# Kernel optimization log

Measured on AMD Instinct MI355X. Metric: run time of the kernel, lower is better.

## Reference

```python
import jax, jax.numpy as jnp
import numpy as np

B, T, D, E, K = 4, 2048, 1024, 8, 2

def setup_inputs() -> dict:
    key = jax.random.key(0)
    ks = jax.random.split(key, 4)
    scale = 1.0 / np.sqrt(D)
    return {
        "input_feat": jax.random.normal(ks[0], (B, T, D), dtype=jnp.float32),
        "delta": jax.random.normal(ks[1], (B, T, D), dtype=jnp.float32),
        "gate_W": jax.random.normal(ks[2], (E, D), dtype=jnp.float32) * scale,
        "gate_b": jnp.zeros((E,), dtype=jnp.float32),
        "expert_W": jax.random.normal(ks[3], (E, D, D), dtype=jnp.float32) * scale,
        "expert_b": jnp.zeros((E, D), dtype=jnp.float32),
    }

def reference(input_feat, delta, gate_W, gate_b, expert_W, expert_b):
    # Gating: logits [B,T,E], top-k over experts, softmax over the k logits
    gate_logits = jnp.einsum("btd,ed->bte", input_feat, gate_W) + gate_b
    topk_vals, topk_idx = jax.lax.top_k(gate_logits, K)          # [B,T,K]
    topk_weights = jax.nn.softmax(topk_vals, axis=-1)            # [B,T,K]

    # Dense per-expert linear on delta: [B,T,D,E] (torch Linear: x @ W.T + b)
    expert_outputs = jnp.einsum("btd,efd->btfe", delta, expert_W) + expert_b.T

    # Gather top-k expert outputs and weighted-combine
    idx = jnp.broadcast_to(topk_idx[:, :, None, :], (B, T, D, K))
    topk_outputs = jnp.take_along_axis(expert_outputs, idx, axis=-1)  # [B,T,D,K]
    weighted_output = jnp.sum(topk_outputs * topk_weights[:, :, None, :], axis=-1)
    return weighted_output
```

## Files before the change

kernel.cpp:

```cpp
#include <hip/hip_runtime.h>
#include <stdint.h>

#define NTOK 8192
#define D 1024
#define E 8
#define BM 128
#define BN 64
#define BK 64

typedef __attribute__((ext_vector_type(8))) short short8;
typedef __attribute__((ext_vector_type(4))) float f32x4;

__device__ __forceinline__ ushort f2bf(float f) {
  uint32_t x = __float_as_uint(f);
  x += 0x7FFFu + ((x >> 16) & 1u);
  return (ushort)(x >> 16);
}

#define NW4 2097152
#define ND4 2097152
#define NO4 2097152
__global__ __launch_bounds__(256) void convert_zero_kernel(
    const float* __restrict__ expert_W, const float* __restrict__ delta,
    ushort* __restrict__ Wb, ushort* __restrict__ Db,
    float* __restrict__ out, int* __restrict__ cnt) {
  int i = blockIdx.x * 256 + threadIdx.x;
  if (i < E) cnt[i] = 0;
  if (i < NW4) {
    float4 v = ((const float4*)expert_W)[i];
    ushort4 u; u.x = f2bf(v.x); u.y = f2bf(v.y); u.z = f2bf(v.z); u.w = f2bf(v.w);
    ((ushort4*)Wb)[i] = u;
  } else if (i < NW4 + ND4) {
    int j = i - NW4;
    float4 v = ((const float4*)delta)[j];
    ushort4 u; u.x = f2bf(v.x); u.y = f2bf(v.y); u.z = f2bf(v.z); u.w = f2bf(v.w);
    ((ushort4*)Db)[j] = u;
  } else {
    int j = i - NW4 - ND4;
    ((float4*)out)[j] = (float4){0.f, 0.f, 0.f, 0.f};
  }
}

__global__ __launch_bounds__(256) void gate_topk_kernel(
    const float* __restrict__ x, const float* __restrict__ gW,
    const float* __restrict__ gb,
    int* __restrict__ idx01, float2* __restrict__ w01) {
  int wave = threadIdx.x >> 6;
  int lane = threadIdx.x & 63;
  int t = blockIdx.x * 4 + wave;

  const float4* xr = (const float4*)(x + (size_t)t * D) + lane * 4;
  float acc[E];
#pragma unroll
  for (int e = 0; e < E; ++e) acc[e] = 0.f;
#pragma unroll
  for (int q = 0; q < 4; ++q) {
    float4 xv = xr[q];
#pragma unroll
    for (int e = 0; e < E; ++e) {
      float4 wv = ((const float4*)(gW + e * D))[lane * 4 + q];
      acc[e] += xv.x * wv.x + xv.y * wv.y + xv.z * wv.z + xv.w * wv.w;
    }
  }
#pragma unroll
  for (int e = 0; e < E; ++e) {
    float v = acc[e];
#pragma unroll
    for (int off = 32; off > 0; off >>= 1) v += __shfl_xor(v, off, 64);
    acc[e] = v;
  }
  if (lane == 0) {
    float lg[E];
#pragma unroll
    for (int e = 0; e < E; ++e) lg[e] = acc[e] + gb[e];
    int i0 = 0; float v0 = lg[0];
#pragma unroll
    for (int e = 1; e < E; ++e) { if (lg[e] > v0) { v0 = lg[e]; i0 = e; } }
    int i1 = -1; float v1 = -1e30f;
#pragma unroll
    for (int e = 0; e < E; ++e) { if (e != i0 && lg[e] > v1) { v1 = lg[e]; i1 = e; } }
    float e1 = __expf(v1 - v0);
    float inv = 1.f / (1.f + e1);
    idx01[t] = i0 | (i1 << 16);
    w01[t] = make_float2(inv, e1 * inv);
  }
}

__global__ __launch_bounds__(256) void bin_kernel(
    const int* __restrict__ idx01, const float2* __restrict__ w01,
    int* __restrict__ cnt, int* __restrict__ list, float* __restrict__ wlist) {
  __shared__ int hist[E];
  __shared__ int base[E];
  int tid = threadIdx.x;
  int t = blockIdx.x * 256 + tid;
  if (tid < E) hist[tid] = 0;
  __syncthreads();

  int packed = idx01[t];
  float2 w = w01[t];
  int i0 = packed & 0xFFFF, i1 = packed >> 16;
  int r0 = atomicAdd(&hist[i0], 1);
  int r1 = atomicAdd(&hist[i1], 1);
  __syncthreads();
  if (tid < E) base[tid] = atomicAdd(&cnt[tid], hist[tid]);
  __syncthreads();

  int s0 = base[i0] + r0;
  list[i0 * NTOK + s0] = t; wlist[i0 * NTOK + s0] = w.x;
  int s1 = base[i1] + r1;
  list[i1 * NTOK + s1] = t; wlist[i1 * NTOK + s1] = w.y;
}

__global__ __launch_bounds__(256) void moe_gemm_kernel(
    const ushort* __restrict__ Db, const ushort* __restrict__ Wb,
    const float* __restrict__ eb, const int* __restrict__ cnt,
    const int* __restrict__ list, const float* __restrict__ wlist,
    float* __restrict__ out) {
  int bx = blockIdx.x;
  int mt = bx >> 7;
  int rem = bx & 127;
  int e = rem >> 4;
  int nt = rem & 15;
  int M = cnt[e];
  int m0 = mt * BM;
  if (m0 >= M) return;
  int n0 = nt * BN;

  __shared__ ushort As[BM * BK];
  __shared__ ushort Bs[BN * BK];

  int tid = threadIdx.x;
  int wave = tid >> 6;
  int lane = tid & 63;
  int wm = wave >> 1;
  int wn = wave & 1;
  const int c = lane & 15;
  const int q = lane >> 4;

  const int* listE = list + e * NTOK;

  int rloc = lane >> 3;
  int gglob = (lane & 7) ^ rloc;
  const ushort* aptr[4];
  ushort* alds[4];
#pragma unroll
  for (int p = 0; p < 4; ++p) {
    int r = m0 + wave * 32 + p * 8 + rloc;
    int tok = listE[r < M ? r : m0];
    aptr[p] = Db + (size_t)tok * D + gglob * 8;
    alds[p] = &As[(wave * 32 + p * 8) * BK];
  }
  const ushort* WbE = Wb + ((size_t)e << 20);
  const ushort* bptr[2];
  ushort* blds[2];
#pragma unroll
  for (int sub = 0; sub < 2; ++sub) {
    int row = n0 + wave * 16 + sub * 8 + rloc;
    bptr[sub] = WbE + (size_t)row * D + gglob * 8;
    blds[sub] = &Bs[(wave * 16 + sub * 8) * BK];
  }

  f32x4 acc[4][2];
#pragma unroll
  for (int i = 0; i < 4; ++i)
#pragma unroll
    for (int j = 0; j < 2; ++j)
      acc[i][j] = (f32x4){0.f, 0.f, 0.f, 0.f};

  for (int k0 = 0; k0 < D; k0 += BK) {
#pragma unroll
    for (int p = 0; p < 4; ++p)
      __builtin_amdgcn_global_load_lds(
          (const __attribute__((address_space(1))) void*)(aptr[p] + k0),
          (__attribute__((address_space(3))) void*)alds[p], 16, 0, 0);
#pragma unroll
    for (int sub = 0; sub < 2; ++sub)
      __builtin_amdgcn_global_load_lds(
          (const __attribute__((address_space(1))) void*)(bptr[sub] + k0),
          (__attribute__((address_space(3))) void*)blds[sub], 16, 0, 0);
    __syncthreads();

#pragma unroll
    for (int s = 0; s < 2; ++s) {
      int sw = (((s * 4 + q) ^ (c & 7)) * 8);
      short8 a[4], b[2];
#pragma unroll
      for (int i = 0; i < 4; ++i)
        a[i] = *(const short8*)&As[(wm * 64 + i * 16 + c) * BK + sw];
#pragma unroll
      for (int j = 0; j < 2; ++j)
        b[j] = *(const short8*)&Bs[(wn * 32 + j * 16 + c) * BK + sw];
#pragma unroll
      for (int i = 0; i < 4; ++i)
#pragma unroll
        for (int j = 0; j < 2; ++j)
          acc[i][j] = __builtin_amdgcn_mfma_f32_16x16x32_bf16(a[i], b[j], acc[i][j], 0, 0, 0);
    }
    __syncthreads();
  }

  float bias[2];
#pragma unroll
  for (int j = 0; j < 2; ++j)
    bias[j] = eb[e * D + n0 + wn * 32 + j * 16 + c];
  const float* wlE = wlist + e * NTOK;
#pragma unroll
  for (int i = 0; i < 4; ++i) {
#pragma unroll
    for (int r = 0; r < 4; ++r) {
      int m = m0 + wm * 64 + i * 16 + q * 4 + r;
      if (m < M) {
        int tok = listE[m];
        float w = wlE[m];
        float* orow = out + (size_t)tok * D + n0 + wn * 32 + c;
#pragma unroll
        for (int j = 0; j < 2; ++j)
          atomicAdd(&orow[j * 16], (acc[i][j][r] + bias[j]) * w);
      }
    }
  }
}

extern "C" void kernel_launch(void* const* d_in, const int* in_sizes, int n_in,
                              void* d_out, int out_size, void* d_ws, size_t ws_size,
                              hipStream_t stream) {
  const float* input_feat = (const float*)d_in[0];
  const float* delta      = (const float*)d_in[1];
  const float* gate_W     = (const float*)d_in[2];
  const float* gate_b     = (const float*)d_in[3];
  const float* expert_W   = (const float*)d_in[4];
  const float* expert_b   = (const float*)d_in[5];
  float* out = (float*)d_out;

  char* ws = (char*)d_ws;
  ushort* Wb    = (ushort*)ws;
  ushort* Db    = (ushort*)(ws + 16777216);
  char*   meta  = ws + 2 * 16777216;
  int*    cnt   = (int*)meta;
  int*    list  = (int*)(meta + 256);
  float*  wlist = (float*)(meta + 256 + NTOK * E * 4);
  int*    idx01 = (int*)(meta + 256 + 2 * NTOK * E * 4);
  float2* w01   = (float2*)(meta + 256 + 2 * NTOK * E * 4 + NTOK * 4);

  int total4 = NW4 + ND4 + NO4;
  convert_zero_kernel<<<total4 / 256, 256, 0, stream>>>(expert_W, delta, Wb, Db, out, cnt);
  gate_topk_kernel<<<NTOK / 4, 256, 0, stream>>>(input_feat, gate_W, gate_b, idx01, w01);
  bin_kernel<<<NTOK / 256, 256, 0, stream>>>(idx01, w01, cnt, list, wlist);
  moe_gemm_kernel<<<(NTOK / BM) * 128, 256, 0, stream>>>(
      Db, Wb, expert_b, cnt, list, wlist, out);
}
```

Measured before the change: 236.8 us.

## Widen GEMM N-tile to 128, fuse convert and gate kernels, reorder block mapping

New measurement: 266.5 us. 1.13x slower.

```diff
diff --git a/kernel.cpp b/kernel.cpp
--- a/kernel.cpp
+++ b/kernel.cpp
@@ -5,7 +5,7 @@
 #define D 1024
 #define E 8
 #define BM 128
-#define BN 64
+#define BN 128
 #define BK 64
 
 typedef __attribute__((ext_vector_type(8))) short short8;
@@ -20,34 +20,37 @@
 #define NW4 2097152
 #define ND4 2097152
 #define NO4 2097152
-__global__ __launch_bounds__(256) void convert_zero_kernel(
+#define CONV_BLOCKS ((NW4 + ND4 + NO4) / 256)
+#define GATE_BLOCKS (NTOK / 4)
+
+__global__ __launch_bounds__(256) void fused_pre_kernel(
     const float* __restrict__ expert_W, const float* __restrict__ delta,
-    ushort* __restrict__ Wb, ushort* __restrict__ Db,
-    float* __restrict__ out, int* __restrict__ cnt) {
-  int i = blockIdx.x * 256 + threadIdx.x;
-  if (i < E) cnt[i] = 0;
-  if (i < NW4) {
-    float4 v = ((const float4*)expert_W)[i];
-    ushort4 u; u.x = f2bf(v.x); u.y = f2bf(v.y); u.z = f2bf(v.z); u.w = f2bf(v.w);
-    ((ushort4*)Wb)[i] = u;
-  } else if (i < NW4 + ND4) {
-    int j = i - NW4;
-    float4 v = ((const float4*)delta)[j];
-    ushort4 u; u.x = f2bf(v.x); u.y = f2bf(v.y); u.z = f2bf(v.z); u.w = f2bf(v.w);
-    ((ushort4*)Db)[j] = u;
-  } else {
-    int j = i - NW4 - ND4;
-    ((float4*)out)[j] = (float4){0.f, 0.f, 0.f, 0.f};
-  }
-}
-
-__global__ __launch_bounds__(256) void gate_topk_kernel(
     const float* __restrict__ x, const float* __restrict__ gW,
     const float* __restrict__ gb,
+    ushort* __restrict__ Wb, ushort* __restrict__ Db,
+    float* __restrict__ out, int* __restrict__ cnt,
     int* __restrict__ idx01, float2* __restrict__ w01) {
+  int b = blockIdx.x;
+  if (b < CONV_BLOCKS) {
+    int i = b * 256 + threadIdx.x;
+    if (i < E) cnt[i] = 0;
+    if (i < NW4) {
+      float4 v = ((const float4*)expert_W)[i];
+      ushort4 u; u.x = f2bf(v.x); u.y = f2bf(v.y); u.z = f2bf(v.z); u.w = f2bf(v.w);
+      ((ushort4*)Wb)[i] = u;
+    } else if (i < NW4 + ND4) {
+      int j = i - NW4;
+      float4 v = ((const float4*)delta)[j];
+      ushort4 u; u.x = f2bf(v.x); u.y = f2bf(v.y); u.z = f2bf(v.z); u.w = f2bf(v.w);
+      ((ushort4*)Db)[j] = u;
+    } else {
+      ((float4*)out)[i - NW4 - ND4] = (float4){0.f, 0.f, 0.f, 0.f};
+    }
+    return;
+  }
   int wave = threadIdx.x >> 6;
   int lane = threadIdx.x & 63;
-  int t = blockIdx.x * 4 + wave;
+  int t = (b - CONV_BLOCKS) * 4 + wave;
 
   const float4* xr = (const float4*)(x + (size_t)t * D) + lane * 4;
   float acc[E];
@@ -111,16 +114,15 @@
   list[i1 * NTOK + s1] = t; wlist[i1 * NTOK + s1] = w.y;
 }
 
-__global__ __launch_bounds__(256) void moe_gemm_kernel(
+__global__ __launch_bounds__(256, 4) void moe_gemm_kernel(
     const ushort* __restrict__ Db, const ushort* __restrict__ Wb,
     const float* __restrict__ eb, const int* __restrict__ cnt,
     const int* __restrict__ list, const float* __restrict__ wlist,
     float* __restrict__ out) {
   int bx = blockIdx.x;
-  int mt = bx >> 7;
-  int rem = bx & 127;
-  int e = rem >> 4;
-  int nt = rem & 15;
+  int e = bx & 7;
+  int nt = (bx >> 3) & 7;
+  int mt = bx >> 6;
   int M = cnt[e];
   int m0 = mt * BM;
   if (m0 >= M) return;
@@ -151,20 +153,20 @@
     alds[p] = &As[(wave * 32 + p * 8) * BK];
   }
   const ushort* WbE = Wb + ((size_t)e << 20);
-  const ushort* bptr[2];
-  ushort* blds[2];
-#pragma unroll
-  for (int sub = 0; sub < 2; ++sub) {
-    int row = n0 + wave * 16 + sub * 8 + rloc;
-    bptr[sub] = WbE + (size_t)row * D + gglob * 8;
-    blds[sub] = &Bs[(wave * 16 + sub * 8) * BK];
-  }
-
-  f32x4 acc[4][2];
+  const ushort* bptr[4];
+  ushort* blds[4];
+#pragma unroll
+  for (int p = 0; p < 4; ++p) {
+    int row = n0 + wave * 32 + p * 8 + rloc;
+    bptr[p] = WbE + (size_t)row * D + gglob * 8;
+    blds[p] = &Bs[(wave * 32 + p * 8) * BK];
+  }
+
+  f32x4 acc[4][4];
 #pragma unroll
   for (int i = 0; i < 4; ++i)
 #pragma unroll
-    for (int j = 0; j < 2; ++j)
+    for (int j = 0; j < 4; ++j)
       acc[i][j] = (f32x4){0.f, 0.f, 0.f, 0.f};
 
   for (int k0 = 0; k0 < D; k0 += BK) {
@@ -174,35 +176,35 @@
           (const __attribute__((address_space(1))) void*)(aptr[p] + k0),
           (__attribute__((address_space(3))) void*)alds[p], 16, 0, 0);
 #pragma unroll
-    for (int sub = 0; sub < 2; ++sub)
+    for (int p = 0; p < 4; ++p)
       __builtin_amdgcn_global_load_lds(
-          (const __attribute__((address_space(1))) void*)(bptr[sub] + k0),
-          (__attribute__((address_space(3))) void*)blds[sub], 16, 0, 0);
+          (const __attribute__((address_space(1))) void*)(bptr[p] + k0),
+          (__attribute__((address_space(3))) void*)blds[p], 16, 0, 0);
     __syncthreads();
 
 #pragma unroll
     for (int s = 0; s < 2; ++s) {
       int sw = (((s * 4 + q) ^ (c & 7)) * 8);
-      short8 a[4], b[2];
+      short8 a[4], b[4];
 #pragma unroll
       for (int i = 0; i < 4; ++i)
         a[i] = *(const short8*)&As[(wm * 64 + i * 16 + c) * BK + sw];
 #pragma unroll
-      for (int j = 0; j < 2; ++j)
-        b[j] = *(const short8*)&Bs[(wn * 32 + j * 16 + c) * BK + sw];
+      for (int j = 0; j < 4; ++j)
+        b[j] = *(const short8*)&Bs[(wn * 64 + j * 16 + c) * BK + sw];
 #pragma unroll
       for (int i = 0; i < 4; ++i)
 #pragma unroll
-        for (int j = 0; j < 2; ++j)
+        for (int j = 0; j < 4; ++j)
           acc[i][j] = __builtin_amdgcn_mfma_f32_16x16x32_bf16(a[i], b[j], acc[i][j], 0, 0, 0);
     }
     __syncthreads();
   }
 
-  float bias[2];
-#pragma unroll
-  for (int j = 0; j < 2; ++j)
-    bias[j] = eb[e * D + n0 + wn * 32 + j * 16 + c];
+  float bias[4];
+#pragma unroll
+  for (int j = 0; j < 4; ++j)
+    bias[j] = eb[e * D + n0 + wn * 64 + j * 16 + c];
   const float* wlE = wlist + e * NTOK;
 #pragma unroll
   for (int i = 0; i < 4; ++i) {
@@ -212,9 +214,9 @@
       if (m < M) {
         int tok = listE[m];
         float w = wlE[m];
-        float* orow = out + (size_t)tok * D + n0 + wn * 32 + c;
-#pragma unroll
-        for (int j = 0; j < 2; ++j)
+        float* orow = out + (size_t)tok * D + n0 + wn * 64 + c;
+#pragma unroll
+        for (int j = 0; j < 4; ++j)
           atomicAdd(&orow[j * 16], (acc[i][j][r] + bias[j]) * w);
       }
     }
@@ -242,10 +244,9 @@
   int*    idx01 = (int*)(meta + 256 + 2 * NTOK * E * 4);
   float2* w01   = (float2*)(meta + 256 + 2 * NTOK * E * 4 + NTOK * 4);
 
-  int total4 = NW4 + ND4 + NO4;
-  convert_zero_kernel<<<total4 / 256, 256, 0, stream>>>(expert_W, delta, Wb, Db, out, cnt);
-  gate_topk_kernel<<<NTOK / 4, 256, 0, stream>>>(input_feat, gate_W, gate_b, idx01, w01);
+  fused_pre_kernel<<<CONV_BLOCKS + GATE_BLOCKS, 256, 0, stream>>>(
+      expert_W, delta, input_feat, gate_W, gate_b, Wb, Db, out, cnt, idx01, w01);
   bin_kernel<<<NTOK / 256, 256, 0, stream>>>(idx01, w01, cnt, list, wlist);
-  moe_gemm_kernel<<<(NTOK / BM) * 128, 256, 0, stream>>>(
+  moe_gemm_kernel<<<(NTOK / BM) * 64, 256, 0, stream>>>(
       Db, Wb, expert_b, cnt, list, wlist, out);
 }
```
